# Kernel optimization log

Measured on AMD Instinct MI355X. Metric: run time of the kernel, lower is better.

Reference implementation:

```python
import jax, jax.numpy as jnp
import numpy as np

N_USERS = 100000
N_ITEMS = 50000
N_NODES = N_USERS + N_ITEMS
N_EDGES = 4800000
EMB_DIM = 64
N_LAYERS = 3


def setup_inputs() -> dict:
    key = jax.random.key(0)
    k1, k2, k3, k4, k5 = jax.random.split(key, 5)
    user_emb = jax.random.normal(k1, (N_USERS, EMB_DIM), dtype=jnp.float32)
    item_emb = jax.random.normal(k2, (N_ITEMS, EMB_DIM), dtype=jnp.float32)
    # COO representation of the (symmetric-normalized) adjacency matrix
    edge_src = jax.random.randint(k3, (N_EDGES,), 0, N_NODES, dtype=jnp.int32)
    edge_dst = jax.random.randint(k4, (N_EDGES,), 0, N_NODES, dtype=jnp.int32)
    edge_weight = jax.random.uniform(k5, (N_EDGES,), dtype=jnp.float32)
    return {
        "user_emb": user_emb,
        "item_emb": item_emb,
        "edge_weight": edge_weight,
        "edge_src": edge_src,
        "edge_dst": edge_dst,
    }


def _spmm(edge_src, edge_dst, edge_weight, x):
    # out[i] = sum_j A[i, j] * x[j]  with A in COO (dst=row i, src=col j)
    msgs = edge_weight[:, None] * x[edge_src]  # [E, D]
    return jax.ops.segment_sum(msgs, edge_dst, num_segments=N_NODES)


def reference(user_emb, item_emb, edge_weight, edge_src, edge_dst):
    ego = jnp.concatenate([user_emb, item_emb], axis=0)  # [N, D]
    acc = ego  # running sum over layer embeddings (layer 0 included)
    for _ in range(N_LAYERS):
        ego = _spmm(edge_src, edge_dst, edge_weight, ego)
        acc = acc + ego
    mean_emb = acc / jnp.float32(N_LAYERS + 1)  # mean over (L+1) layers
    new_user = mean_emb[:N_USERS]
    new_item = mean_emb[N_USERS:]
    return new_user, new_item
```

## Files before the change

### kernel.cpp

```cpp
#include <hip/hip_runtime.h>
#include <hip/hip_fp16.h>

#define N_USERS 100000
#define N_ITEMS 50000
#define N_NODES 150000
#define N_EDGES 4800000
#define EMB 64
#define N_LAYERS 3

#define NBKT 256
#define NPB  586
#define NREP 8
#define SUBCAP 2624
#define CAP (NREP * SUBCAP)
#define P1GRID 2344
#define INITGRID 9375

typedef unsigned int u32;
typedef unsigned short u16;
typedef u32 vu4 __attribute__((ext_vector_type(4)));
typedef u32 vu2 __attribute__((ext_vector_type(2)));
typedef float vf4 __attribute__((ext_vector_type(4)));

#define W_BITS 14
#define W_SCALE 16384.0f
#define W_INV   (1.0f / 16384.0f)
#define W_MASK  16383u

__device__ __forceinline__ float hh(u16 v) {
    return __half2float(__ushort_as_half(v));
}

__global__ __launch_bounds__(256) void k_build1(const int4*   __restrict__ src4,
                                                const int4*   __restrict__ dst4,
                                                const float4* __restrict__ w4,
                                                int* __restrict__ cursor,
                                                u32* __restrict__ pk_arr,
                                                u16* __restrict__ ld_arr,
                                                const float4* __restrict__ user,
                                                const float4* __restrict__ item,
                                                ushort4* __restrict__ h0) {
    int tid = threadIdx.x;

    if (blockIdx.x >= P1GRID) {
        int i = (int)(blockIdx.x - P1GRID) * 256 + tid;
        const int total4 = N_NODES * EMB / 4;
        const int user4  = N_USERS * EMB / 4;
        if (i >= total4) return;
        float4 v = (i < user4) ? user[i] : item[i - user4];
        ushort4 h;
        h.x = __half_as_ushort(__float2half_rn(v.x));
        h.y = __half_as_ushort(__float2half_rn(v.y));
        h.z = __half_as_ushort(__float2half_rn(v.z));
        h.w = __half_as_ushort(__float2half_rn(v.w));
        h0[i] = h;
        return;
    }

    __shared__ int hist[NBKT];
    __shared__ int base[NBKT];
    __shared__ int bscan[NBKT];
    __shared__ u32 s_pk[2048];
    __shared__ u32 s_meta[2048];
    hist[tid] = 0;
    __syncthreads();

    int g0 = blockIdx.x * 512 + tid * 2;
    bool act = (g0 < N_EDGES / 4);

    u32 pk[8];
    u32 meta[8];
    int rk[8];
    if (act) {
        int4 d0 = dst4[g0], d1 = dst4[g0 + 1];
        int4 s0 = src4[g0], s1 = src4[g0 + 1];
        float4 f0 = w4[g0], f1 = w4[g0 + 1];
        int   ds[8] = {d0.x, d0.y, d0.z, d0.w, d1.x, d1.y, d1.z, d1.w};
        int   ss[8] = {s0.x, s0.y, s0.z, s0.w, s1.x, s1.y, s1.z, s1.w};
        float wf[8] = {f0.x, f0.y, f0.z, f0.w, f1.x, f1.y, f1.z, f1.w};
        #pragma unroll
        for (int k = 0; k < 8; ++k) {
            u32 d  = (u32)ds[k];
            u32 b  = d / NPB;
            u32 ld = d - b * NPB;
            rk[k]  = atomicAdd(&hist[b], 1);
            u32 wq = (u32)(wf[k] * W_SCALE + 0.5f);
            if (wq > W_MASK) wq = W_MASK;
            pk[k]   = ((u32)ss[k] << W_BITS) | wq;
            meta[k] = (b << 10) | ld;
        }
    }
    __syncthreads();

    int rep = blockIdx.x & (NREP - 1);
    int h = hist[tid];
    if (h > 0) base[tid] = atomicAdd(&cursor[rep * NBKT + tid], h);
    bscan[tid] = h;
    __syncthreads();
    for (int off = 1; off < NBKT; off <<= 1) {
        int t = 0;
        if (tid >= off) t = bscan[tid - off];
        __syncthreads();
        if (tid >= off) bscan[tid] += t;
        __syncthreads();
    }

    if (act) {
        #pragma unroll
        for (int k = 0; k < 8; ++k) {
            u32 b = meta[k] >> 10;
            int s = (bscan[b] - hist[b]) + rk[k];
            s_pk[s]   = pk[k];
            s_meta[s] = meta[k];
        }
    }
    __syncthreads();

    int total = bscan[NBKT - 1];
    #pragma unroll
    for (int k = 0; k < 8; ++k) {
        int s = k * 256 + tid;
        if (s < total) {
            u32 mt = s_meta[s];
            u32 b  = mt >> 10;
            int pos = base[b] + (s - (bscan[b] - hist[b]));
            if (pos < SUBCAP) {
                size_t slot = (size_t)b * CAP + (size_t)rep * SUBCAP + pos;
                pk_arr[slot] = s_pk[s];
                ld_arr[slot] = (u16)(mt & 1023u);
            }
        }
    }
}

extern __shared__ u32 s_pk2[];

__global__ __launch_bounds__(1024) void k_p2(const int* __restrict__ cursor,
                                             const u32* __restrict__ pk_arr,
                                             const u16* __restrict__ ld_arr,
                                             int* __restrict__ row_ptr,
                                             u32* __restrict__ pairs) {
    __shared__ int hist[1024];
    __shared__ int start[NPB];
    __shared__ int btot[NBKT];
    __shared__ int bsum[NBKT];
    int b = blockIdx.x;
    int tid = threadIdx.x;
    hist[tid] = 0;
    if (tid < NBKT) {
        int s = 0;
        #pragma unroll
        for (int r = 0; r < NREP; ++r) s += cursor[r * NBKT + tid];
        btot[tid] = s;
        bsum[tid] = s;
    }
    if (b == 0 && tid == 0) row_ptr[N_NODES] = N_EDGES;
    __syncthreads();
    for (int off = 1; off < NBKT; off <<= 1) {
        int t = 0;
        if (tid < NBKT && tid >= off) t = bsum[tid - off];
        __syncthreads();
        if (tid < NBKT && tid >= off) bsum[tid] += t;
        __syncthreads();
    }
    int gbase = bsum[b] - btot[b];

    int lo = b * NPB;
    int nbn = N_NODES - lo; if (nbn > NPB) nbn = NPB;

    int n[NREP];
    #pragma unroll
    for (int r = 0; r < NREP; ++r) {
        int c = cursor[r * NBKT + b];
        n[r] = (c > SUBCAP) ? SUBCAP : c;
    }

    for (int r = 0; r < NREP; ++r) {
        const u16* p = ld_arr + (size_t)b * CAP + (size_t)r * SUBCAP;
        for (int i = tid; i < n[r]; i += 1024)
            atomicAdd(&hist[p[i]], 1);
    }
    __syncthreads();

    int val = hist[tid];
    for (int off = 1; off < 1024; off <<= 1) {
        int t = 0;
        if (tid >= off) t = hist[tid - off];
        __syncthreads();
        if (tid >= off) hist[tid] += t;
        __syncthreads();
    }
    int excl = hist[tid] - val;
    if (tid < nbn) row_ptr[lo + tid] = gbase + excl;
    if (tid < NPB) start[tid] = excl;
    __syncthreads();

    for (int r = 0; r < NREP; ++r) {
        const u16* p = ld_arr + (size_t)b * CAP + (size_t)r * SUBCAP;
        const u32* q = pk_arr + (size_t)b * CAP + (size_t)r * SUBCAP;
        for (int i = tid; i < n[r]; i += 1024) {
            int slot = atomicAdd(&start[p[i]], 1);
            s_pk2[slot] = q[i];
        }
    }
    __syncthreads();

    int total = hist[1023];
    for (int s = tid; s < total; s += 1024)
        pairs[gbase + s] = s_pk2[s];
}

struct Dec4 { u32 r0, r1, r2, r3; float w0, w1, w2, w3; };

__device__ __forceinline__ Dec4 dec_fast(vu4 p) {
    Dec4 d;
    d.r0 = p.x >> W_BITS; d.w0 = (float)(p.x & W_MASK);
    d.r1 = p.y >> W_BITS; d.w1 = (float)(p.y & W_MASK);
    d.r2 = p.z >> W_BITS; d.w2 = (float)(p.z & W_MASK);
    d.r3 = p.w >> W_BITS; d.w3 = (float)(p.w & W_MASK);
    return d;
}

__device__ __forceinline__ Dec4 dec_mask(vu4 p, int eb, int beg, int end) {
    Dec4 d;
    bool v0 = (eb + 0 >= beg) && (eb + 0 < end);
    bool v1 = (eb + 1 >= beg) && (eb + 1 < end);
    bool v2 = (eb + 2 >= beg) && (eb + 2 < end);
    bool v3 = (eb + 3 >= beg) && (eb + 3 < end);
    d.r0 = v0 ? (p.x >> W_BITS) : 0u; d.w0 = v0 ? (float)(p.x & W_MASK) : 0.f;
    d.r1 = v1 ? (p.y >> W_BITS) : 0u; d.w1 = v1 ? (float)(p.y & W_MASK) : 0.f;
    d.r2 = v2 ? (p.z >> W_BITS) : 0u; d.w2 = v2 ? (float)(p.z & W_MASK) : 0.f;
    d.r3 = v3 ? (p.w >> W_BITS) : 0u; d.w3 = v3 ? (float)(p.w & W_MASK) : 0.f;
    return d;
}

__device__ __forceinline__ Dec4 dec(vu4 p, int lo, int beg, int end, int g) {
    if (lo >= beg && lo + 16 <= end) return dec_fast(p);
    return dec_mask(p, lo + 4 * g, beg, end);
}

__device__ __forceinline__ vu4 ldp(const u32* p) {
    return __builtin_nontemporal_load((const vu4*)p);
}

__device__ __forceinline__ vu2 ldx(const char* xbase, u32 r, u32 moff) {
    return *(const vu2*)(xbase + (size_t)(r * 128u + moff));
}

__device__ __forceinline__ void fmix2(float& a0, float& a1, float w, u32 x) {
    asm("v_fma_mix_f32 %0, %1, %2, %0 op_sel:[0,0,0] op_sel_hi:[0,1,0]"
        : "+v"(a0) : "v"(w), "v"(x));
    asm("v_fma_mix_f32 %0, %1, %2, %0 op_sel:[0,1,0] op_sel_hi:[0,1,0]"
        : "+v"(a1) : "v"(w), "v"(x));
}

__device__ __forceinline__ void acc4(vu2 xv, float w,
                                     float& ax, float& ay, float& az, float& aw) {
    fmix2(ax, ay, w, xv.x);
    fmix2(az, aw, w, xv.y);
}

#define LOADX(pfx, d) \
    vu2 pfx##0 = ldx(xbase, d.r0, moff), pfx##1 = ldx(xbase, d.r1, moff), \
        pfx##2 = ldx(xbase, d.r2, moff), pfx##3 = ldx(xbase, d.r3, moff)
#define ACCX(pfx, d) \
    acc4(pfx##0, d.w0, ax, ay, az, aw); acc4(pfx##1, d.w1, ax, ay, az, aw); \
    acc4(pfx##2, d.w2, ax, ay, az, aw); acc4(pfx##3, d.w3, ax, ay, az, aw)
#define RED(v) v += __shfl_xor(v, 16); v += __shfl_xor(v, 32)

template<int FIN>
__global__ __launch_bounds__(256) void k_gather(const int* __restrict__ row_ptr,
                                                const u32* __restrict__ pairs,
                                                const __half* __restrict__ x,
                                                __half* __restrict__ nxt,
                                                const ushort4* __restrict__ e0,
                                                const ushort4* __restrict__ e1,
                                                const ushort4* __restrict__ e2,
                                                float* __restrict__ outp) {
    int wave = (blockIdx.x * blockDim.x + threadIdx.x) >> 6;
    int lane = threadIdx.x & 63;
    if (wave >= N_NODES) return;

    const int m = lane & 15;
    ushort4 ega = {}, ea = {}, eb = {};
    if (FIN && lane < 16) {
        size_t idx = (size_t)wave * 16 + m;
        ega = e0[idx]; ea = e1[idx]; eb = e2[idx];
    }

    int beg = row_ptr[wave];
    int end = row_ptr[wave + 1];

    const int g = lane >> 4;
    const u32 moff = (u32)m << 3;
    const char* xbase = (const char*)x;

    float ax = 0.f, ay = 0.f, az = 0.f, aw = 0.f;

    int jb = beg & ~3;
    int nb = (end - jb + 15) >> 4;
    const u32* pp = pairs + jb + 4 * g;

    if (nb == 1) {
        vu4 P0 = ldp(pp);
        Dec4 d0 = dec(P0, jb, beg, end, g);
        LOADX(xa, d0);
        ACCX(xa, d0);
    } else if (nb == 2) {
        vu4 P0 = ldp(pp);
        vu4 P1 = ldp(pp + 16);
        Dec4 d0 = dec(P0, jb, beg, end, g);
        LOADX(xa, d0);
        Dec4 d1 = dec(P1, jb + 16, beg, end, g);
        LOADX(xc, d1);
        ACCX(xa, d0);
        ACCX(xc, d1);
    } else if (nb == 3) {
        vu4 P0 = ldp(pp);
        vu4 P1 = ldp(pp + 16);
        vu4 P2 = ldp(pp + 32);
        Dec4 d0 = dec(P0, jb, beg, end, g);
        LOADX(xa, d0);
        Dec4 d1 = dec(P1, jb + 16, beg, end, g);
        LOADX(xc, d1);
        ACCX(xa, d0);
        Dec4 d2 = dec(P2, jb + 32, beg, end, g);
        LOADX(xd, d2);
        ACCX(xc, d1);
        ACCX(xd, d2);
    } else if (nb >= 4) {
        vu4 P0 = ldp(pp);
        vu4 P1 = ldp(pp + 16);
        vu4 P2 = ldp(pp + 32);
        Dec4 d0 = dec(P0, jb, beg, end, g);
        LOADX(xa, d0);
        Dec4 d1 = dec(P1, jb + 16, beg, end, g);
        LOADX(xc, d1);
        ACCX(xa, d0);
        vu4 P3 = ldp(pp + 48);
        Dec4 d2 = dec(P2, jb + 32, beg, end, g);
        LOADX(xd, d2);
        ACCX(xc, d1);
        Dec4 d3 = dec(P3, jb + 48, beg, end, g);
        LOADX(xe, d3);
        ACCX(xd, d2);
        ACCX(xe, d3);
        for (int b = 4; b < nb; ++b) {
            vu4 Pl = ldp(pp + (size_t)16 * b);
            Dec4 dl = dec(Pl, jb + 16 * b, beg, end, g);
            LOADX(xf, dl);
            ACCX(xf, dl);
        }
    }

    RED(ax); RED(ay); RED(az); RED(aw);

    if (lane < 16) {
        if (FIN) {
            vf4 o;
            o.x = (hh(ega.x) + hh(ea.x) + hh(eb.x) + ax * W_INV) * 0.25f;
            o.y = (hh(ega.y) + hh(ea.y) + hh(eb.y) + ay * W_INV) * 0.25f;
            o.z = (hh(ega.z) + hh(ea.z) + hh(eb.z) + az * W_INV) * 0.25f;
            o.w = (hh(ega.w) + hh(ea.w) + hh(eb.w) + aw * W_INV) * 0.25f;
            __builtin_nontemporal_store(o, (vf4*)outp + (size_t)wave * 16 + m);
        } else {
            ushort4 h;
            h.x = __half_as_ushort(__float2half_rn(ax * W_INV));
            h.y = __half_as_ushort(__float2half_rn(ay * W_INV));
            h.z = __half_as_ushort(__float2half_rn(az * W_INV));
            h.w = __half_as_ushort(__float2half_rn(aw * W_INV));
            ((ushort4*)nxt)[(size_t)wave * 16 + m] = h;
        }
    }
}

__global__ void k_spmm(const int*   __restrict__ src,
                       const int*   __restrict__ dst,
                       const float* __restrict__ w,
                       const float* __restrict__ x,
                       float*       __restrict__ y) {
    long long t = (long long)blockIdx.x * blockDim.x + threadIdx.x;
    int e = (int)(t >> 4);
    if (e >= N_EDGES) return;
    int q = (int)(t & 15);
    int   s  = src[e];
    int   d  = dst[e];
    float we = w[e];
    const float4* xs = (const float4*)(x + (long long)s * EMB);
    float4 v = xs[q];
    float* yd = y + (long long)d * EMB + q * 4;
    atomicAdd(yd + 0, we * v.x);
    atomicAdd(yd + 1, we * v.y);
    atomicAdd(yd + 2, we * v.z);
    atomicAdd(yd + 3, we * v.w);
}

__global__ void k_init_f32(const float4* __restrict__ user,
                           const float4* __restrict__ item,
                           float4* __restrict__ out,
                           float4* __restrict__ cur) {
    int i = blockIdx.x * blockDim.x + threadIdx.x;
    const int total4 = N_NODES * EMB / 4;
    const int user4  = N_USERS * EMB / 4;
    if (i >= total4) return;
    float4 v = (i < user4) ? user[i] : item[i - user4];
    out[i] = v;
    cur[i] = v;
}

__global__ void k_acc(float4* __restrict__ out,
                      const float4* __restrict__ buf,
                      float scale) {
    int i = blockIdx.x * blockDim.x + threadIdx.x;
    const int total4 = N_NODES * EMB / 4;
    if (i >= total4) return;
    float4 o = out[i];
    float4 b = buf[i];
    o.x = (o.x + b.x) * scale;
    o.y = (o.y + b.y) * scale;
    o.z = (o.z + b.z) * scale;
    o.w = (o.w + b.w) * scale;
    out[i] = o;
}

extern "C" void kernel_launch(void* const* d_in, const int* in_sizes, int n_in,
                              void* d_out, int out_size, void* d_ws, size_t ws_size,
                              hipStream_t stream) {
    const float* user_emb = (const float*)d_in[0];
    const float* item_emb = (const float*)d_in[1];
    const float* edge_w   = (const float*)d_in[2];
    const int*   edge_src = (const int*)d_in[3];
    const int*   edge_dst = (const int*)d_in[4];
    float* out = (float*)d_out;

    const size_t feat_elems = (size_t)N_NODES * EMB;
    const size_t feat_bytes_f32 = feat_elems * 4;
    const size_t feat_bytes_f16 = feat_elems * 2;

    char* ws = (char*)d_ws;
    size_t off = 0;
    __half* h0 = (__half*)(ws + off); off += feat_bytes_f16;
    __half* h1 = (__half*)(ws + off); off += feat_bytes_f16;
    __half* h2 = (__half*)(ws + off); off += feat_bytes_f16;
    int* row_ptr  = (int*)(ws + off); off += ((size_t)(N_NODES + 1) * 4 + 63) / 64 * 64;
    int* cursor   = (int*)(ws + off); off += (size_t)NREP * NBKT * 4;
    u32* pk_arr = (u32*)(ws + off);   off += (size_t)NBKT * CAP * 4;
    u16* ld_arr = (u16*)(ws + off);   off += (size_t)NBKT * CAP * 2;
    u32* pairs  = (u32*)(ws + off);   off += (size_t)N_EDGES * 4 + 64;
    const size_t needed = off;

    const int block = 256;
    const int total4 = (int)(feat_elems / 4);
    const int fgrid = (total4 + block - 1) / block;
    const int bgrid = P1GRID + INITGRID;
    const int ggrid = (N_NODES + 3) / 4;

    if (ws_size >= needed) {
        (void)hipMemsetAsync(cursor, 0, (size_t)NREP * NBKT * 4, stream);

        k_build1<<<bgrid, block, 0, stream>>>((const int4*)edge_src,
                                              (const int4*)edge_dst,
                                              (const float4*)edge_w,
                                              cursor, pk_arr, ld_arr,
                                              (const float4*)user_emb,
                                              (const float4*)item_emb,
                                              (ushort4*)h0);
        k_p2<<<NBKT, 1024, (size_t)CAP * 4, stream>>>(cursor, pk_arr, ld_arr,
                                                      row_ptr, pairs);

        k_gather<0><<<ggrid, block, 0, stream>>>(row_ptr, pairs, h0, h1,
                                                 nullptr, nullptr, nullptr,
                                                 nullptr);
        k_gather<0><<<ggrid, block, 0, stream>>>(row_ptr, pairs, h1, h2,
                                                 nullptr, nullptr, nullptr,
                                                 nullptr);
        k_gather<1><<<ggrid, block, 0, stream>>>(row_ptr, pairs, h2, nullptr,
                                                 (const ushort4*)h0,
                                                 (const ushort4*)h1,
                                                 (const ushort4*)h2,
                                                 out);
    } else {
        float* buf0 = (float*)d_ws;
        float* buf1 = buf0 + feat_elems;
        k_init_f32<<<fgrid, block, 0, stream>>>((const float4*)user_emb,
                                                (const float4*)item_emb,
                                                (float4*)out, (float4*)buf0);
        float* cur = buf0;
        float* nxt = buf1;
        for (int layer = 0; layer < N_LAYERS; ++layer) {
            (void)hipMemsetAsync(nxt, 0, feat_bytes_f32, stream);
            long long threads = (long long)N_EDGES * 16;
            int grid = (int)((threads + block - 1) / block);
            k_spmm<<<grid, block, 0, stream>>>(edge_src, edge_dst, edge_w, cur, nxt);
            float scale = (layer == N_LAYERS - 1) ? (1.0f / (N_LAYERS + 1)) : 1.0f;
            k_acc<<<fgrid, block, 0, stream>>>((float4*)out, (const float4*)nxt, scale);
            float* tmp = cur; cur = nxt; nxt = tmp;
        }
    }
}
```

Baseline: 416.3 us.

## Fuse first SpMM layer into CSR build kernel using LDS-resident pairs

```diff
diff --git a/kernel.cpp b/kernel.cpp
--- a/kernel.cpp
+++ b/kernel.cpp
@@ -30,6 +30,64 @@
 __device__ __forceinline__ float hh(u16 v) {
     return __half2float(__ushort_as_half(v));
 }
+
+struct Dec4 { u32 r0, r1, r2, r3; float w0, w1, w2, w3; };
+
+__device__ __forceinline__ Dec4 dec_fast(vu4 p) {
+    Dec4 d;
+    d.r0 = p.x >> W_BITS; d.w0 = (float)(p.x & W_MASK);
+    d.r1 = p.y >> W_BITS; d.w1 = (float)(p.y & W_MASK);
+    d.r2 = p.z >> W_BITS; d.w2 = (float)(p.z & W_MASK);
+    d.r3 = p.w >> W_BITS; d.w3 = (float)(p.w & W_MASK);
+    return d;
+}
+
+__device__ __forceinline__ Dec4 dec_mask(vu4 p, int eb, int beg, int end) {
+    Dec4 d;
+    bool v0 = (eb + 0 >= beg) && (eb + 0 < end);
+    bool v1 = (eb + 1 >= beg) && (eb + 1 < end);
+    bool v2 = (eb + 2 >= beg) && (eb + 2 < end);
+    bool v3 = (eb + 3 >= beg) && (eb + 3 < end);
+    d.r0 = v0 ? (p.x >> W_BITS) : 0u; d.w0 = v0 ? (float)(p.x & W_MASK) : 0.f;
+    d.r1 = v1 ? (p.y >> W_BITS) : 0u; d.w1 = v1 ? (float)(p.y & W_MASK) : 0.f;
+    d.r2 = v2 ? (p.z >> W_BITS) : 0u; d.w2 = v2 ? (float)(p.z & W_MASK) : 0.f;
+    d.r3 = v3 ? (p.w >> W_BITS) : 0u; d.w3 = v3 ? (float)(p.w & W_MASK) : 0.f;
+    return d;
+}
+
+__device__ __forceinline__ Dec4 dec(vu4 p, int lo, int beg, int end, int g) {
+    if (lo >= beg && lo + 16 <= end) return dec_fast(p);
+    return dec_mask(p, lo + 4 * g, beg, end);
+}
+
+__device__ __forceinline__ vu4 ldp(const u32* p) {
+    return __builtin_nontemporal_load((const vu4*)p);
+}
+
+__device__ __forceinline__ vu2 ldx(const char* xbase, u32 r, u32 moff) {
+    return *(const vu2*)(xbase + (size_t)(r * 128u + moff));
+}
+
+__device__ __forceinline__ void fmix2(float& a0, float& a1, float w, u32 x) {
+    asm("v_fma_mix_f32 %0, %1, %2, %0 op_sel:[0,0,0] op_sel_hi:[0,1,0]"
+        : "+v"(a0) : "v"(w), "v"(x));
+    asm("v_fma_mix_f32 %0, %1, %2, %0 op_sel:[0,1,0] op_sel_hi:[0,1,0]"
+        : "+v"(a1) : "v"(w), "v"(x));
+}
+
+__device__ __forceinline__ void acc4(vu2 xv, float w,
+                                     float& ax, float& ay, float& az, float& aw) {
+    fmix2(ax, ay, w, xv.x);
+    fmix2(az, aw, w, xv.y);
+}
+
+#define LOADX(pfx, d) \
+    vu2 pfx##0 = ldx(xbase, d.r0, moff), pfx##1 = ldx(xbase, d.r1, moff), \
+        pfx##2 = ldx(xbase, d.r2, moff), pfx##3 = ldx(xbase, d.r3, moff)
+#define ACCX(pfx, d) \
+    acc4(pfx##0, d.w0, ax, ay, az, aw); acc4(pfx##1, d.w1, ax, ay, az, aw); \
+    acc4(pfx##2, d.w2, ax, ay, az, aw); acc4(pfx##3, d.w3, ax, ay, az, aw)
+#define RED(v) v += __shfl_xor(v, 16); v += __shfl_xor(v, 32)
 
 __global__ __launch_bounds__(256) void k_build1(const int4*   __restrict__ src4,
                                                 const int4*   __restrict__ dst4,
@@ -135,13 +193,17 @@
 
 extern __shared__ u32 s_pk2[];
 
-__global__ __launch_bounds__(1024) void k_p2(const int* __restrict__ cursor,
-                                             const u32* __restrict__ pk_arr,
-                                             const u16* __restrict__ ld_arr,
-                                             int* __restrict__ row_ptr,
-                                             u32* __restrict__ pairs) {
+__global__ __launch_bounds__(1024) void k_p2g(const int* __restrict__ cursor,
+                                              const u32* __restrict__ pk_arr,
+                                              const u16* __restrict__ ld_arr,
+                                              int* __restrict__ row_ptr,
+                                              u32* __restrict__ pairs,
+                                              const __half* __restrict__ x,
+                                              __half* __restrict__ nxt) {
     __shared__ int hist[1024];
     __shared__ int start[NPB];
+    __shared__ int rbeg[NPB];
+    __shared__ int rend[NPB];
     __shared__ int btot[NBKT];
     __shared__ int bsum[NBKT];
     int b = blockIdx.x;
@@ -192,7 +254,11 @@
     }
     int excl = hist[tid] - val;
     if (tid < nbn) row_ptr[lo + tid] = gbase + excl;
-    if (tid < NPB) start[tid] = excl;
+    if (tid < NPB) {
+        start[tid] = excl;
+        rbeg[tid]  = excl;
+        rend[tid]  = hist[tid];
+    }
     __syncthreads();
 
     for (int r = 0; r < NREP; ++r) {
@@ -206,67 +272,90 @@
     __syncthreads();
 
     int total = hist[1023];
+    if (tid < 16) s_pk2[total + tid] = 0;
     for (int s = tid; s < total; s += 1024)
         pairs[gbase + s] = s_pk2[s];
-}
-
-struct Dec4 { u32 r0, r1, r2, r3; float w0, w1, w2, w3; };
-
-__device__ __forceinline__ Dec4 dec_fast(vu4 p) {
-    Dec4 d;
-    d.r0 = p.x >> W_BITS; d.w0 = (float)(p.x & W_MASK);
-    d.r1 = p.y >> W_BITS; d.w1 = (float)(p.y & W_MASK);
-    d.r2 = p.z >> W_BITS; d.w2 = (float)(p.z & W_MASK);
-    d.r3 = p.w >> W_BITS; d.w3 = (float)(p.w & W_MASK);
-    return d;
-}
-
-__device__ __forceinline__ Dec4 dec_mask(vu4 p, int eb, int beg, int end) {
-    Dec4 d;
-    bool v0 = (eb + 0 >= beg) && (eb + 0 < end);
-    bool v1 = (eb + 1 >= beg) && (eb + 1 < end);
-    bool v2 = (eb + 2 >= beg) && (eb + 2 < end);
-    bool v3 = (eb + 3 >= beg) && (eb + 3 < end);
-    d.r0 = v0 ? (p.x >> W_BITS) : 0u; d.w0 = v0 ? (float)(p.x & W_MASK) : 0.f;
-    d.r1 = v1 ? (p.y >> W_BITS) : 0u; d.w1 = v1 ? (float)(p.y & W_MASK) : 0.f;
-    d.r2 = v2 ? (p.z >> W_BITS) : 0u; d.w2 = v2 ? (float)(p.z & W_MASK) : 0.f;
-    d.r3 = v3 ? (p.w >> W_BITS) : 0u; d.w3 = v3 ? (float)(p.w & W_MASK) : 0.f;
-    return d;
-}
-
-__device__ __forceinline__ Dec4 dec(vu4 p, int lo, int beg, int end, int g) {
-    if (lo >= beg && lo + 16 <= end) return dec_fast(p);
-    return dec_mask(p, lo + 4 * g, beg, end);
-}
-
-__device__ __forceinline__ vu4 ldp(const u32* p) {
-    return __builtin_nontemporal_load((const vu4*)p);
-}
-
-__device__ __forceinline__ vu2 ldx(const char* xbase, u32 r, u32 moff) {
-    return *(const vu2*)(xbase + (size_t)(r * 128u + moff));
-}
-
-__device__ __forceinline__ void fmix2(float& a0, float& a1, float w, u32 x) {
-    asm("v_fma_mix_f32 %0, %1, %2, %0 op_sel:[0,0,0] op_sel_hi:[0,1,0]"
-        : "+v"(a0) : "v"(w), "v"(x));
-    asm("v_fma_mix_f32 %0, %1, %2, %0 op_sel:[0,1,0] op_sel_hi:[0,1,0]"
-        : "+v"(a1) : "v"(w), "v"(x));
-}
-
-__device__ __forceinline__ void acc4(vu2 xv, float w,
-                                     float& ax, float& ay, float& az, float& aw) {
-    fmix2(ax, ay, w, xv.x);
-    fmix2(az, aw, w, xv.y);
-}
-
-#define LOADX(pfx, d) \
-    vu2 pfx##0 = ldx(xbase, d.r0, moff), pfx##1 = ldx(xbase, d.r1, moff), \
-        pfx##2 = ldx(xbase, d.r2, moff), pfx##3 = ldx(xbase, d.r3, moff)
-#define ACCX(pfx, d) \
-    acc4(pfx##0, d.w0, ax, ay, az, aw); acc4(pfx##1, d.w1, ax, ay, az, aw); \
-    acc4(pfx##2, d.w2, ax, ay, az, aw); acc4(pfx##3, d.w3, ax, ay, az, aw)
-#define RED(v) v += __shfl_xor(v, 16); v += __shfl_xor(v, 32)
+    __syncthreads();
+
+    int wid  = tid >> 6;
+    int lane = tid & 63;
+    const int m = lane & 15;
+    const int g = lane >> 4;
+    const u32 moff = (u32)m << 3;
+    const char* xbase = (const char*)x;
+
+    for (int row = wid; row < nbn; row += 16) {
+        int beg = rbeg[row];
+        int end = rend[row];
+        float ax = 0.f, ay = 0.f, az = 0.f, aw = 0.f;
+        int jb = beg & ~3;
+        int nb = (end - jb + 15) >> 4;
+        const u32* pp = s_pk2 + jb + 4 * g;
+
+        if (nb == 1) {
+            vu4 P0 = *(const vu4*)pp;
+            Dec4 d0 = dec(P0, jb, beg, end, g);
+            LOADX(xa, d0);
+            ACCX(xa, d0);
+        } else if (nb == 2) {
+            vu4 P0 = *(const vu4*)pp;
+            vu4 P1 = *(const vu4*)(pp + 16);
+            Dec4 d0 = dec(P0, jb, beg, end, g);
+            LOADX(xa, d0);
+            Dec4 d1 = dec(P1, jb + 16, beg, end, g);
+            LOADX(xc, d1);
+            ACCX(xa, d0);
+            ACCX(xc, d1);
+        } else if (nb == 3) {
+            vu4 P0 = *(const vu4*)pp;
+            vu4 P1 = *(const vu4*)(pp + 16);
+            vu4 P2 = *(const vu4*)(pp + 32);
+            Dec4 d0 = dec(P0, jb, beg, end, g);
+            LOADX(xa, d0);
+            Dec4 d1 = dec(P1, jb + 16, beg, end, g);
+            LOADX(xc, d1);
+            ACCX(xa, d0);
+            Dec4 d2 = dec(P2, jb + 32, beg, end, g);
+            LOADX(xd, d2);
+            ACCX(xc, d1);
+            ACCX(xd, d2);
+        } else if (nb >= 4) {
+            vu4 P0 = *(const vu4*)pp;
+            vu4 P1 = *(const vu4*)(pp + 16);
+            vu4 P2 = *(const vu4*)(pp + 32);
+            Dec4 d0 = dec(P0, jb, beg, end, g);
+            LOADX(xa, d0);
+            Dec4 d1 = dec(P1, jb + 16, beg, end, g);
+            LOADX(xc, d1);
+            ACCX(xa, d0);
+            vu4 P3 = *(const vu4*)(pp + 48);
+            Dec4 d2 = dec(P2, jb + 32, beg, end, g);
+            LOADX(xd, d2);
+            ACCX(xc, d1);
+            Dec4 d3 = dec(P3, jb + 48, beg, end, g);
+            LOADX(xe, d3);
+            ACCX(xd, d2);
+            ACCX(xe, d3);
+            for (int t = 4; t < nb; ++t) {
+                vu4 Pl = *(const vu4*)(pp + (size_t)16 * t);
+                Dec4 dl = dec(Pl, jb + 16 * t, beg, end, g);
+                LOADX(xf, dl);
+                ACCX(xf, dl);
+            }
+        }
+
+        RED(ax); RED(ay); RED(az); RED(aw);
+
+        if (lane < 16) {
+            ushort4 h;
+            h.x = __half_as_ushort(__float2half_rn(ax * W_INV));
+            h.y = __half_as_ushort(__float2half_rn(ay * W_INV));
+            h.z = __half_as_ushort(__float2half_rn(az * W_INV));
+            h.w = __half_as_ushort(__float2half_rn(aw * W_INV));
+            ((ushort4*)nxt)[(size_t)(lo + row) * 16 + m] = h;
+        }
+    }
+}
 
 template<int FIN>
 __global__ __launch_bounds__(256) void k_gather(const int* __restrict__ row_ptr,
@@ -345,9 +434,9 @@
         LOADX(xe, d3);
         ACCX(xd, d2);
         ACCX(xe, d3);
-        for (int b = 4; b < nb; ++b) {
-            vu4 Pl = ldp(pp + (size_t)16 * b);
-            Dec4 dl = dec(Pl, jb + 16 * b, beg, end, g);
+        for (int t = 4; t < nb; ++t) {
+            vu4 Pl = ldp(pp + (size_t)16 * t);
+            Dec4 dl = dec(Pl, jb + 16 * t, beg, end, g);
             LOADX(xf, dl);
             ACCX(xf, dl);
         }
@@ -465,12 +554,10 @@
                                               (const float4*)user_emb,
                                               (const float4*)item_emb,
                                               (ushort4*)h0);
-        k_p2<<<NBKT, 1024, (size_t)CAP * 4, stream>>>(cursor, pk_arr, ld_arr,
-                                                      row_ptr, pairs);
-
-        k_gather<0><<<ggrid, block, 0, stream>>>(row_ptr, pairs, h0, h1,
-                                                 nullptr, nullptr, nullptr,
-                                                 nullptr);
+        k_p2g<<<NBKT, 1024, (size_t)(CAP + 16) * 4, stream>>>(cursor, pk_arr,
+                                                              ld_arr, row_ptr,
+                                                              pairs, h0, h1);
+
         k_gather<0><<<ggrid, block, 0, stream>>>(row_ptr, pairs, h1, h2,
                                                  nullptr, nullptr, nullptr,
                                                  nullptr);
```

New measurement: 417.2 us. About the same (+0.2%).
